# Kernel tuning notes

Measured on AMD Instinct MI355X. Metric: run time of the kernel, lower is better.

Reference implementation:

```python
import jax, jax.numpy as jnp
import numpy as np

D_MODEL = 1024
N_HEAD = 16
HEAD_DIM = D_MODEL // N_HEAD
B, S = 4, 2048


def setup_inputs() -> dict:
    key = jax.random.key(0)
    ks = jax.random.split(key, 11)
    scale = 1.0 / np.sqrt(D_MODEL)
    inp = {
        "q": jax.random.normal(ks[0], (B, S, D_MODEL), jnp.float32),
        "k": jax.random.normal(ks[1], (B, S, D_MODEL), jnp.float32),
        "v": jax.random.normal(ks[2], (B, S, D_MODEL), jnp.float32),
        # torch nn.Linear weights: [out_features, in_features], y = x @ W.T + b
        "Wq": jax.random.normal(ks[3], (D_MODEL, D_MODEL), jnp.float32) * scale,
        "bq": jax.random.normal(ks[4], (D_MODEL,), jnp.float32) * scale,
        "Wk": jax.random.normal(ks[5], (D_MODEL, D_MODEL), jnp.float32) * scale,
        "bk": jax.random.normal(ks[6], (D_MODEL,), jnp.float32) * scale,
        "Wv": jax.random.normal(ks[7], (D_MODEL, D_MODEL), jnp.float32) * scale,
        "bv": jax.random.normal(ks[8], (D_MODEL,), jnp.float32) * scale,
        "Wo": jax.random.normal(ks[9], (D_MODEL, D_MODEL), jnp.float32) * scale,
        "bo": jax.random.normal(ks[10], (D_MODEL,), jnp.float32) * scale,
    }
    return inp


def _split_heads(x):
    # [B, S, D] -> [B, H, S, hd]
    b, s, _ = x.shape
    return x.reshape(b, s, N_HEAD, HEAD_DIM).transpose(0, 2, 1, 3)


def reference(q, k, v, Wq, bq, Wk, bk, Wv, bv, Wo, bo):
    qh = _split_heads(q @ Wq.T + bq)
    kh = _split_heads(k @ Wk.T + bk)
    vh = _split_heads(v @ Wv.T + bv)
    scores = jnp.einsum("bhqd,bhkd->bhqk", qh, kh) / jnp.sqrt(
        jnp.asarray(HEAD_DIM, qh.dtype)
    )
    weights = jax.nn.softmax(scores, axis=-1)  # [B, H, Sq, Sk]
    ctx = jnp.einsum("bhqk,bhkd->bhqd", weights, vh)
    b, h, s, d = ctx.shape
    ctx = ctx.transpose(0, 2, 1, 3).reshape(b, s, h * d)  # [B, S, D]
    return ctx @ Wo.T + bo
```

## Files before the change

kernel.cpp:

```cpp
#include <hip/hip_runtime.h>
#include <hip/hip_bf16.h>

typedef float   f32x4   __attribute__((ext_vector_type(4)));
typedef __bf16  bf16x8  __attribute__((ext_vector_type(8)));
typedef unsigned short u16x8 __attribute__((ext_vector_type(8)));
typedef unsigned short u16x4 __attribute__((ext_vector_type(4)));

#define DEVI __device__ __forceinline__

DEVI unsigned short f2bf_bits(float f) {
    __bf16 h = (__bf16)f;
    return __builtin_bit_cast(unsigned short, h);
}

DEVI f32x4 mfma_bf16(bf16x8 a, bf16x8 b, f32x4 c) {
    return __builtin_amdgcn_mfma_f32_16x16x32_bf16(a, b, c, 0, 0, 0);
}

DEVI float fast_exp2(float x) {
#if __has_builtin(__builtin_amdgcn_exp2f)
    return __builtin_amdgcn_exp2f(x);
#else
    float r;
    asm("v_exp_f32 %0, %1" : "=v"(r) : "v"(x));
    return r;
#endif
}

DEVI void gload16(const void* g, void* l) {
    __builtin_amdgcn_global_load_lds(
        (const __attribute__((address_space(1))) void*)g,
        (__attribute__((address_space(3))) void*)l, 16, 0, 0);
}

__global__ __launch_bounds__(256) void convert_w_kernel(
    const float* __restrict__ Wq, const float* __restrict__ Wk,
    const float* __restrict__ Wv, unsigned short* __restrict__ Wb)
{
    int idx = blockIdx.x * 256 + threadIdx.x;
    int which = idx >> 17;
    int off = (idx & 131071) * 8;
    const float* src = which == 0 ? Wq : (which == 1 ? Wk : Wv);
    f32x4 a = *(const f32x4*)(src + off);
    f32x4 b = *(const f32x4*)(src + off + 4);
    u16x8 h;
#pragma unroll
    for (int j = 0; j < 4; ++j) { h[j] = f2bf_bits(a[j]); h[4 + j] = f2bf_bits(b[j]); }
    *(u16x8*)(Wb + (size_t)which * 1048576 + off) = h;
}

template <bool A_ASYNC, bool OUT_F32>
__global__ __launch_bounds__(256) void gemm_bt_kernel(
    const void* __restrict__ Ap, const void* __restrict__ Wp,
    const float* __restrict__ bias, void* __restrict__ Cp,
    int M, int N, int K, float scale)
{
    __shared__ __align__(16) char ldsA[128 * 128];
    __shared__ __align__(16) char ldsB[128 * 128];
    const int t = threadIdx.x;
    const int wave = t >> 6, lane = t & 63;
    const int g = lane >> 4, c = lane & 15;
    const int rowbase = blockIdx.x * 128;
    const int colbase = blockIdx.y * 128;
    const int wr = (wave >> 1) * 64, wc = (wave & 1) * 64;

    const int arow = lane >> 3;
    const int aslot = (lane & 7) ^ arow;

    const float* fbase[4];
#pragma unroll
    for (int ch = 0; ch < 4; ++ch) {
        int id = ch * 256 + t;
        int row = id >> 3;
        int col = (id & 7) * 8;
        if constexpr (A_ASYNC)
            fbase[ch] = (const float*)Wp + (size_t)(colbase + row) * K + col;
        else
            fbase[ch] = (const float*)Ap + (size_t)(rowbase + row) * K + col;
    }

    f32x4 pre0[4], pre1[4];
#pragma unroll
    for (int ch = 0; ch < 4; ++ch) {
        pre0[ch] = *(const f32x4*)(fbase[ch]);
        pre1[ch] = *(const f32x4*)(fbase[ch] + 4);
    }

    f32x4 acc[4][4] = {};

    for (int kt = 0; kt < K; kt += 64) {
        if constexpr (A_ASYNC) {
            const unsigned short* Ab = (const unsigned short*)Ap;
#pragma unroll
            for (int j = 0; j < 4; ++j) {
                int rg = wave * 4 + j;
                int row = rg * 8 + arow;
                gload16(Ab + (size_t)(rowbase + row) * K + kt + aslot * 8,
                        ldsA + rg * 1024);
            }
        } else {
            const unsigned short* Wb = (const unsigned short*)Wp;
#pragma unroll
            for (int j = 0; j < 4; ++j) {
                int rg = wave * 4 + j;
                int row = rg * 8 + arow;
                gload16(Wb + (size_t)(colbase + row) * K + kt + aslot * 8,
                        ldsB + rg * 1024);
            }
        }

#pragma unroll
        for (int ch = 0; ch < 4; ++ch) {
            int id = ch * 256 + t;
            int row = id >> 3;
            int col = (id & 7) * 8;
            int dst = row * 128 + ((col * 2) ^ ((row & 7) << 4));
            u16x8 hv;
#pragma unroll
            for (int j = 0; j < 4; ++j) { hv[j] = f2bf_bits(pre0[ch][j]); hv[4 + j] = f2bf_bits(pre1[ch][j]); }
            if constexpr (A_ASYNC)
                *(u16x8*)(ldsB + dst) = hv;
            else
                *(u16x8*)(ldsA + dst) = hv;
        }
        __syncthreads();

        if (kt + 64 < K) {
#pragma unroll
            for (int ch = 0; ch < 4; ++ch) {
                pre0[ch] = *(const f32x4*)(fbase[ch] + kt + 64);
                pre1[ch] = *(const f32x4*)(fbase[ch] + kt + 68);
            }
        }

#pragma unroll
        for (int kk = 0; kk < 2; ++kk) {
            bf16x8 af[4], bfr[4];
#pragma unroll
            for (int i = 0; i < 4; ++i) {
                int ra = wr + i * 16 + c;
                af[i] = *(const bf16x8*)(ldsA + ra * 128 + ((kk * 64 + g * 16) ^ ((ra & 7) << 4)));
                int rb = wc + i * 16 + c;
                bfr[i] = *(const bf16x8*)(ldsB + rb * 128 + ((kk * 64 + g * 16) ^ ((rb & 7) << 4)));
            }
#pragma unroll
            for (int i = 0; i < 4; ++i)
#pragma unroll
                for (int j = 0; j < 4; ++j)
                    acc[i][j] = mfma_bf16(af[i], bfr[j], acc[i][j]);
        }
        __syncthreads();
    }

#pragma unroll
    for (int j = 0; j < 4; ++j) {
        int coln = colbase + wc + j * 16 + c;
        float bv = bias[coln];
#pragma unroll
        for (int i = 0; i < 4; ++i) {
            int row0 = rowbase + wr + i * 16 + g * 4;
#pragma unroll
            for (int r = 0; r < 4; ++r) {
                float val = (acc[i][j][r] + bv) * scale;
                if constexpr (OUT_F32)
                    ((float*)Cp)[(size_t)(row0 + r) * N + coln] = val;
                else
                    ((unsigned short*)Cp)[(size_t)(row0 + r) * N + coln] = f2bf_bits(val);
            }
        }
    }
}

__global__ __launch_bounds__(256) void transpose_v_kernel(
    const unsigned short* __restrict__ Vp, unsigned short* __restrict__ Vt)
{
    __shared__ unsigned short tile[64][72];
    const int t = threadIdx.x;
    const int bh = blockIdx.y, b = bh >> 4, h = bh & 15;
    const int s0 = blockIdx.x * 64;
#pragma unroll
    for (int ch = 0; ch < 2; ++ch) {
        int id = ch * 256 + t;
        int srow = id >> 3, dcol = (id & 7) * 8;
        u16x8 v = *(const u16x8*)(Vp + (size_t)(b * 2048 + s0 + srow) * 1024 + h * 64 + dcol);
        *(u16x8*)&tile[srow][dcol] = v;
    }
    __syncthreads();
#pragma unroll
    for (int ch = 0; ch < 2; ++ch) {
        int id = ch * 256 + t;
        int drow = id >> 3, scol = (id & 7) * 8;
        u16x8 ov;
#pragma unroll
        for (int j = 0; j < 8; ++j) ov[j] = tile[scol + j][drow];
        *(u16x8*)(Vt + (size_t)(bh * 64 + drow) * 2048 + s0 + scol) = ov;
    }
}

__global__ __launch_bounds__(256) void attn_kernel(
    const unsigned short* __restrict__ Qp, const unsigned short* __restrict__ Kp,
    const unsigned short* __restrict__ Vt, unsigned short* __restrict__ ctx)
{
    __shared__ __align__(16) char ldsK[64 * 128];
    __shared__ __align__(16) char ldsV[64 * 128];
    __shared__ __align__(16) char ldsP[4][2][16 * 128];
    const int t = threadIdx.x;
    const int wave = t >> 6, lane = t & 63;
    const int g = lane >> 4, c = lane & 15;
    const int bh = blockIdx.y, b = bh >> 4, h = bh & 15;
    const int qb = blockIdx.x * 128;

    bf16x8 qf0[2], qf1[2];
    {
        const unsigned short* q0 = Qp + (size_t)(b * 2048 + qb + wave * 32 + c) * 1024 + h * 64;
        qf0[0] = *(const bf16x8*)(q0 + 8 * g);
        qf0[1] = *(const bf16x8*)(q0 + 32 + 8 * g);
        const unsigned short* q1 = q0 + (size_t)16 * 1024;
        qf1[0] = *(const bf16x8*)(q1 + 8 * g);
        qf1[1] = *(const bf16x8*)(q1 + 32 + 8 * g);
    }

    f32x4 o0[4] = {}, o1[4] = {};
    float psum0 = 0.f, psum1 = 0.f;

    const int row0 = t >> 3, colB = (t & 7) * 8;
    const int row1 = 32 + row0;
    const int dst0 = row0 * 128 + ((colB * 2) ^ ((row0 & 7) << 4));
    const int dst1 = row1 * 128 + ((colB * 2) ^ ((row1 & 7) << 4));
    const unsigned short* Ksrc = Kp + (size_t)(b * 2048) * 1024 + h * 64;
    const unsigned short* Vsrc = Vt + (size_t)(bh * 64) * 2048;

    u16x8 kv0 = *(const u16x8*)(Ksrc + (size_t)row0 * 1024 + colB);
    u16x8 kv1 = *(const u16x8*)(Ksrc + (size_t)row1 * 1024 + colB);
    u16x8 vv0 = *(const u16x8*)(Vsrc + (size_t)row0 * 2048 + colB);
    u16x8 vv1 = *(const u16x8*)(Vsrc + (size_t)row1 * 2048 + colB);

    char* pw0 = ldsP[wave][0];
    char* pw1 = ldsP[wave][1];

    for (int kb = 0; kb < 2048; kb += 64) {
        *(u16x8*)(ldsK + dst0) = kv0;
        *(u16x8*)(ldsK + dst1) = kv1;
        *(u16x8*)(ldsV + dst0) = vv0;
        *(u16x8*)(ldsV + dst1) = vv1;
        __syncthreads();

        if (kb + 64 < 2048) {
            kv0 = *(const u16x8*)(Ksrc + (size_t)(kb + 64 + row0) * 1024 + colB);
            kv1 = *(const u16x8*)(Ksrc + (size_t)(kb + 64 + row1) * 1024 + colB);
            vv0 = *(const u16x8*)(Vsrc + (size_t)row0 * 2048 + kb + 64 + colB);
            vv1 = *(const u16x8*)(Vsrc + (size_t)row1 * 2048 + kb + 64 + colB);
        }

        f32x4 s0[4] = {}, s1[4] = {};
#pragma unroll
        for (int kk = 0; kk < 2; ++kk) {
            bf16x8 kf[4];
#pragma unroll
            for (int ti = 0; ti < 4; ++ti) {
                int rk = ti * 16 + c;
                kf[ti] = *(const bf16x8*)(ldsK + rk * 128 + ((kk * 64 + g * 16) ^ ((rk & 7) << 4)));
            }
#pragma unroll
            for (int ti = 0; ti < 4; ++ti) {
                s0[ti] = mfma_bf16(kf[ti], qf0[kk], s0[ti]);
                s1[ti] = mfma_bf16(kf[ti], qf1[kk], s1[ti]);
            }
        }

#pragma unroll
        for (int ti = 0; ti < 4; ++ti) {
            float p0 = fast_exp2(s0[ti][0]);
            float p1 = fast_exp2(s0[ti][1]);
            float p2 = fast_exp2(s0[ti][2]);
            float p3 = fast_exp2(s0[ti][3]);
            psum0 += (p0 + p1) + (p2 + p3);
            u16x4 hp;
            hp[0] = f2bf_bits(p0); hp[1] = f2bf_bits(p1);
            hp[2] = f2bf_bits(p2); hp[3] = f2bf_bits(p3);
            *(u16x4*)(pw0 + c * 128 + ((ti * 32 + g * 8) ^ ((c & 7) << 4))) = hp;
        }
#pragma unroll
        for (int ti = 0; ti < 4; ++ti) {
            float p0 = fast_exp2(s1[ti][0]);
            float p1 = fast_exp2(s1[ti][1]);
            float p2 = fast_exp2(s1[ti][2]);
            float p3 = fast_exp2(s1[ti][3]);
            psum1 += (p0 + p1) + (p2 + p3);
            u16x4 hp;
            hp[0] = f2bf_bits(p0); hp[1] = f2bf_bits(p1);
            hp[2] = f2bf_bits(p2); hp[3] = f2bf_bits(p3);
            *(u16x4*)(pw1 + c * 128 + ((ti * 32 + g * 8) ^ ((c & 7) << 4))) = hp;
        }

#pragma unroll
        for (int kk = 0; kk < 2; ++kk) {
            bf16x8 vf[4];
#pragma unroll
            for (int ti = 0; ti < 4; ++ti) {
                int rv = ti * 16 + c;
                vf[ti] = *(const bf16x8*)(ldsV + rv * 128 + ((kk * 64 + g * 16) ^ ((rv & 7) << 4)));
            }
            bf16x8 pa0 = *(const bf16x8*)(pw0 + c * 128 + ((kk * 64 + g * 16) ^ ((c & 7) << 4)));
            bf16x8 pa1 = *(const bf16x8*)(pw1 + c * 128 + ((kk * 64 + g * 16) ^ ((c & 7) << 4)));
#pragma unroll
            for (int ti = 0; ti < 4; ++ti) {
                o0[ti] = mfma_bf16(pa0, vf[ti], o0[ti]);
                o1[ti] = mfma_bf16(pa1, vf[ti], o1[ti]);
            }
        }
        __syncthreads();
    }

    psum0 += __shfl_xor(psum0, 16);
    psum0 += __shfl_xor(psum0, 32);
    psum1 += __shfl_xor(psum1, 16);
    psum1 += __shfl_xor(psum1, 32);

#pragma unroll
    for (int r = 0; r < 4; ++r) {
        float inv0 = 1.0f / __shfl(psum0, 4 * g + r);
        float inv1 = 1.0f / __shfl(psum1, 4 * g + r);
        int row0q = qb + wave * 32 + 4 * g + r;
        int row1q = row0q + 16;
#pragma unroll
        for (int ti = 0; ti < 4; ++ti) {
            int col = h * 64 + ti * 16 + c;
            ctx[(size_t)(b * 2048 + row0q) * 1024 + col] = f2bf_bits(o0[ti][r] * inv0);
            ctx[(size_t)(b * 2048 + row1q) * 1024 + col] = f2bf_bits(o1[ti][r] * inv1);
        }
    }
}

extern "C" void kernel_launch(void* const* d_in, const int* in_sizes, int n_in,
                              void* d_out, int out_size, void* d_ws, size_t ws_size,
                              hipStream_t stream)
{
    const float* q  = (const float*)d_in[0];
    const float* k  = (const float*)d_in[1];
    const float* v  = (const float*)d_in[2];
    const float* Wq = (const float*)d_in[3];
    const float* bq = (const float*)d_in[4];
    const float* Wk = (const float*)d_in[5];
    const float* bk = (const float*)d_in[6];
    const float* Wv = (const float*)d_in[7];
    const float* bv = (const float*)d_in[8];
    const float* Wo = (const float*)d_in[9];
    const float* bo = (const float*)d_in[10];
    float* out = (float*)d_out;

    char* ws = (char*)d_ws;
    const size_t SZ = (size_t)8192 * 1024 * 2;
    unsigned short* Qp = (unsigned short*)(ws);
    unsigned short* Kp = (unsigned short*)(ws + SZ);
    unsigned short* Vp = (unsigned short*)(ws + 2 * SZ);
    unsigned short* Vt = (unsigned short*)(ws + 3 * SZ);
    unsigned short* ctx = Vp;
    unsigned short* Wbf = Vt;

    const float QSCALE = 0.1803368801111244f;

    convert_w_kernel<<<dim3(1536), 256, 0, stream>>>(Wq, Wk, Wv, Wbf);

    dim3 gg(64, 8);
    gemm_bt_kernel<false, false><<<gg, 256, 0, stream>>>(q, Wbf,           bq, Qp, 8192, 1024, 1024, QSCALE);
    gemm_bt_kernel<false, false><<<gg, 256, 0, stream>>>(k, Wbf + 1048576, bk, Kp, 8192, 1024, 1024, 1.0f);
    gemm_bt_kernel<false, false><<<gg, 256, 0, stream>>>(v, Wbf + 2097152, bv, Vp, 8192, 1024, 1024, 1.0f);
    transpose_v_kernel<<<dim3(32, 64), 256, 0, stream>>>(Vp, Vt);
    attn_kernel<<<dim3(16, 64), 256, 0, stream>>>(Qp, Kp, Vt, ctx);
    gemm_bt_kernel<true, true><<<gg, 256, 0, stream>>>(ctx, Wo, bo, out, 8192, 1024, 1024, 1.0f);
}
```

Before: 222.4 us.

## Double attention query tile per block to 256 rows, 64 per wave

Result: no change. 224.8 us (+1.1%).

```diff
diff --git a/kernel.cpp b/kernel.cpp
--- a/kernel.cpp
+++ b/kernel.cpp
@@ -203,25 +203,23 @@
 {
     __shared__ __align__(16) char ldsK[64 * 128];
     __shared__ __align__(16) char ldsV[64 * 128];
-    __shared__ __align__(16) char ldsP[4][2][16 * 128];
+    __shared__ __align__(16) char ldsP[4][4][16 * 128];
     const int t = threadIdx.x;
     const int wave = t >> 6, lane = t & 63;
     const int g = lane >> 4, c = lane & 15;
     const int bh = blockIdx.y, b = bh >> 4, h = bh & 15;
-    const int qb = blockIdx.x * 128;
-
-    bf16x8 qf0[2], qf1[2];
-    {
-        const unsigned short* q0 = Qp + (size_t)(b * 2048 + qb + wave * 32 + c) * 1024 + h * 64;
-        qf0[0] = *(const bf16x8*)(q0 + 8 * g);
-        qf0[1] = *(const bf16x8*)(q0 + 32 + 8 * g);
-        const unsigned short* q1 = q0 + (size_t)16 * 1024;
-        qf1[0] = *(const bf16x8*)(q1 + 8 * g);
-        qf1[1] = *(const bf16x8*)(q1 + 32 + 8 * g);
-    }
-
-    f32x4 o0[4] = {}, o1[4] = {};
-    float psum0 = 0.f, psum1 = 0.f;
+    const int qb = blockIdx.x * 256;
+
+    bf16x8 qf[4][2];
+#pragma unroll
+    for (int qs = 0; qs < 4; ++qs) {
+        const unsigned short* q0 = Qp + (size_t)(b * 2048 + qb + wave * 64 + qs * 16 + c) * 1024 + h * 64;
+        qf[qs][0] = *(const bf16x8*)(q0 + 8 * g);
+        qf[qs][1] = *(const bf16x8*)(q0 + 32 + 8 * g);
+    }
+
+    f32x4 o[4][4] = {};
+    float psum[4] = {0.f, 0.f, 0.f, 0.f};
 
     const int row0 = t >> 3, colB = (t & 7) * 8;
     const int row1 = 32 + row0;
@@ -235,9 +233,6 @@
     u16x8 vv0 = *(const u16x8*)(Vsrc + (size_t)row0 * 2048 + colB);
     u16x8 vv1 = *(const u16x8*)(Vsrc + (size_t)row1 * 2048 + colB);
 
-    char* pw0 = ldsP[wave][0];
-    char* pw1 = ldsP[wave][1];
-
     for (int kb = 0; kb < 2048; kb += 64) {
         *(u16x8*)(ldsK + dst0) = kv0;
         *(u16x8*)(ldsK + dst1) = kv1;
@@ -252,7 +247,7 @@
             vv1 = *(const u16x8*)(Vsrc + (size_t)row1 * 2048 + kb + 64 + colB);
         }
 
-        f32x4 s0[4] = {}, s1[4] = {};
+        f32x4 s[4][4] = {};
 #pragma unroll
         for (int kk = 0; kk < 2; ++kk) {
             bf16x8 kf[4];
@@ -262,35 +257,27 @@
                 kf[ti] = *(const bf16x8*)(ldsK + rk * 128 + ((kk * 64 + g * 16) ^ ((rk & 7) << 4)));
             }
 #pragma unroll
+            for (int qs = 0; qs < 4; ++qs)
+#pragma unroll
+                for (int ti = 0; ti < 4; ++ti)
+                    s[qs][ti] = mfma_bf16(kf[ti], qf[qs][kk], s[qs][ti]);
+        }
+
+#pragma unroll
+        for (int qs = 0; qs < 4; ++qs) {
+            char* pw = ldsP[wave][qs];
+#pragma unroll
             for (int ti = 0; ti < 4; ++ti) {
-                s0[ti] = mfma_bf16(kf[ti], qf0[kk], s0[ti]);
-                s1[ti] = mfma_bf16(kf[ti], qf1[kk], s1[ti]);
-            }
-        }
-
-#pragma unroll
-        for (int ti = 0; ti < 4; ++ti) {
-            float p0 = fast_exp2(s0[ti][0]);
-            float p1 = fast_exp2(s0[ti][1]);
-            float p2 = fast_exp2(s0[ti][2]);
-            float p3 = fast_exp2(s0[ti][3]);
-            psum0 += (p0 + p1) + (p2 + p3);
-            u16x4 hp;
-            hp[0] = f2bf_bits(p0); hp[1] = f2bf_bits(p1);
-            hp[2] = f2bf_bits(p2); hp[3] = f2bf_bits(p3);
-            *(u16x4*)(pw0 + c * 128 + ((ti * 32 + g * 8) ^ ((c & 7) << 4))) = hp;
-        }
-#pragma unroll
-        for (int ti = 0; ti < 4; ++ti) {
-            float p0 = fast_exp2(s1[ti][0]);
-            float p1 = fast_exp2(s1[ti][1]);
-            float p2 = fast_exp2(s1[ti][2]);
-            float p3 = fast_exp2(s1[ti][3]);
-            psum1 += (p0 + p1) + (p2 + p3);
-            u16x4 hp;
-            hp[0] = f2bf_bits(p0); hp[1] = f2bf_bits(p1);
-            hp[2] = f2bf_bits(p2); hp[3] = f2bf_bits(p3);
-            *(u16x4*)(pw1 + c * 128 + ((ti * 32 + g * 8) ^ ((c & 7) << 4))) = hp;
+                float p0 = fast_exp2(s[qs][ti][0]);
+                float p1 = fast_exp2(s[qs][ti][1]);
+                float p2 = fast_exp2(s[qs][ti][2]);
+                float p3 = fast_exp2(s[qs][ti][3]);
+                psum[qs] += (p0 + p1) + (p2 + p3);
+                u16x4 hp;
+                hp[0] = f2bf_bits(p0); hp[1] = f2bf_bits(p1);
+                hp[2] = f2bf_bits(p2); hp[3] = f2bf_bits(p3);
+                *(u16x4*)(pw + c * 128 + ((ti * 32 + g * 8) ^ ((c & 7) << 4))) = hp;
+            }
         }
 
 #pragma unroll
@@ -301,33 +288,31 @@
                 int rv = ti * 16 + c;
                 vf[ti] = *(const bf16x8*)(ldsV + rv * 128 + ((kk * 64 + g * 16) ^ ((rv & 7) << 4)));
             }
-            bf16x8 pa0 = *(const bf16x8*)(pw0 + c * 128 + ((kk * 64 + g * 16) ^ ((c & 7) << 4)));
-            bf16x8 pa1 = *(const bf16x8*)(pw1 + c * 128 + ((kk * 64 + g * 16) ^ ((c & 7) << 4)));
+#pragma unroll
+            for (int qs = 0; qs < 4; ++qs) {
+                bf16x8 pa = *(const bf16x8*)(ldsP[wave][qs] + c * 128 + ((kk * 64 + g * 16) ^ ((c & 7) << 4)));
+#pragma unroll
+                for (int ti = 0; ti < 4; ++ti)
+                    o[qs][ti] = mfma_bf16(pa, vf[ti], o[qs][ti]);
+            }
+        }
+        __syncthreads();
+    }
+
+#pragma unroll
+    for (int qs = 0; qs < 4; ++qs) {
+        float ps = psum[qs];
+        ps += __shfl_xor(ps, 16);
+        ps += __shfl_xor(ps, 32);
+#pragma unroll
+        for (int r = 0; r < 4; ++r) {
+            float inv = 1.0f / __shfl(ps, 4 * g + r);
+            int row = qb + wave * 64 + qs * 16 + 4 * g + r;
 #pragma unroll
             for (int ti = 0; ti < 4; ++ti) {
-                o0[ti] = mfma_bf16(pa0, vf[ti], o0[ti]);
-                o1[ti] = mfma_bf16(pa1, vf[ti], o1[ti]);
-            }
-        }
-        __syncthreads();
-    }
-
-    psum0 += __shfl_xor(psum0, 16);
-    psum0 += __shfl_xor(psum0, 32);
-    psum1 += __shfl_xor(psum1, 16);
-    psum1 += __shfl_xor(psum1, 32);
-
-#pragma unroll
-    for (int r = 0; r < 4; ++r) {
-        float inv0 = 1.0f / __shfl(psum0, 4 * g + r);
-        float inv1 = 1.0f / __shfl(psum1, 4 * g + r);
-        int row0q = qb + wave * 32 + 4 * g + r;
-        int row1q = row0q + 16;
-#pragma unroll
-        for (int ti = 0; ti < 4; ++ti) {
-            int col = h * 64 + ti * 16 + c;
-            ctx[(size_t)(b * 2048 + row0q) * 1024 + col] = f2bf_bits(o0[ti][r] * inv0);
-            ctx[(size_t)(b * 2048 + row1q) * 1024 + col] = f2bf_bits(o1[ti][r] * inv1);
+                int col = h * 64 + ti * 16 + c;
+                ctx[(size_t)(b * 2048 + row) * 1024 + col] = f2bf_bits(o[qs][ti][r] * inv);
+            }
         }
     }
 }
@@ -367,6 +352,6 @@
     gemm_bt_kernel<false, false><<<gg, 256, 0, stream>>>(k, Wbf + 1048576, bk, Kp, 8192, 1024, 1024, 1.0f);
     gemm_bt_kernel<false, false><<<gg, 256, 0, stream>>>(v, Wbf + 2097152, bv, Vp, 8192, 1024, 1024, 1.0f);
     transpose_v_kernel<<<dim3(32, 64), 256, 0, stream>>>(Vp, Vt);
-    attn_kernel<<<dim3(16, 64), 256, 0, stream>>>(Qp, Kp, Vt, ctx);
+    attn_kernel<<<dim3(8, 64), 256, 0, stream>>>(Qp, Kp, Vt, ctx);
     gemm_bt_kernel<true, true><<<gg, 256, 0, stream>>>(ctx, Wo, bo, out, 8192, 1024, 1024, 1.0f);
 }
```
